# Performance work log

Hardware: AMD Instinct MI355X
Metric: run time of the kernel (lower is better)

The kernel has to match this reference:

```python
import jax, jax.numpy as jnp
import numpy as np

# ---- piecewise-linear surrogate tables (constants of the surrogate ops) ----
_N = 512
_GX = np.linspace(-10.0, 10.0, _N).astype(np.float32)
_GY = (0.5 * _GX * (1.0 + np.tanh(np.sqrt(2.0 / np.pi) * (_GX + 0.044715 * _GX ** 3)))).astype(np.float32)
_EX = np.linspace(-30.0, 0.0, _N).astype(np.float32)
_EY = np.exp(_EX).astype(np.float32)
_IX = np.geomspace(1e-3, 4096.0, _N).astype(np.float32)
_IY = (1.0 / _IX).astype(np.float32)
_RX = np.geomspace(1e-6, 100.0, _N).astype(np.float32)
_RY = (1.0 / np.sqrt(_RX)).astype(np.float32)

GX, GY = jnp.asarray(_GX), jnp.asarray(_GY)
EX, EY = jnp.asarray(_EX), jnp.asarray(_EY)
IX, IY = jnp.asarray(_IX), jnp.asarray(_IY)
RX, RY = jnp.asarray(_RX), jnp.asarray(_RY)

EXP_CLIP_MIN = -30.0
LN_EPS = 1e-5
N_HEAD = 16

pwl_gelu = lambda x: jnp.interp(x, GX, GY)
pwl_exp = lambda x: jnp.interp(x, EX, EY)
pwl_inv = lambda x: jnp.interp(x, IX, IY)
pwl_rsqrt = lambda x: jnp.interp(x, RX, RY)


def _layernorm_approx(x, w, b):
    mu = jnp.mean(x, axis=-1, keepdims=True)
    xc = x - mu
    var = jnp.mean(xc * xc, axis=-1, keepdims=True)
    inv_std = pwl_rsqrt(var + LN_EPS)
    return xc * inv_std * w + b


def _attn_approx(x, c_attn_w, c_attn_b, c_proj_w, c_proj_b):
    B, T, D = x.shape
    hd = D // N_HEAD
    scale = 1.0 / jnp.sqrt(jnp.float32(hd))
    qkv = x @ c_attn_w + c_attn_b                      # [B,T,3D]
    q, k, v = jnp.split(qkv, 3, axis=-1)
    q = q.reshape(B, T, N_HEAD, hd).transpose(0, 2, 1, 3)  # [B,H,T,hd]
    k = k.reshape(B, T, N_HEAD, hd).transpose(0, 2, 1, 3)
    v = v.reshape(B, T, N_HEAD, hd).transpose(0, 2, 1, 3)
    scores = jnp.einsum('bhqd,bhkd->bhqk', q, k) * scale    # [B,H,T,T]
    causal = jnp.tril(jnp.ones((T, T), dtype=bool))
    scores = jnp.where(causal, scores, -jnp.inf)
    m = jnp.max(scores, axis=-1, keepdims=True)
    s = jnp.clip(scores - m, EXP_CLIP_MIN, 0.0)             # masked -> -30
    e = pwl_exp(s)
    p = e * pwl_inv(jnp.sum(e, axis=-1, keepdims=True))
    out = jnp.einsum('bhqk,bhkd->bhqd', p, v)
    out = out.transpose(0, 2, 1, 3).reshape(B, T, D)
    return out @ c_proj_w + c_proj_b


def _mlp_approx(x, fc_w, fc_b, proj_w, proj_b):
    h = pwl_gelu(x @ fc_w + fc_b)
    return h @ proj_w + proj_b


def setup_inputs() -> dict:
    key = jax.random.key(0)
    ks = jax.random.split(key, 8)
    B, T, D = 2, 1024, 2048
    DF = 4 * D
    w = 0.02
    return {
        'x': jax.random.normal(ks[0], (B, T, D), jnp.float32),
        'ln_1_w': jnp.ones((D,), jnp.float32),
        'ln_1_b': jnp.zeros((D,), jnp.float32),
        'ln_2_w': jnp.ones((D,), jnp.float32),
        'ln_2_b': jnp.zeros((D,), jnp.float32),
        'c_attn_w': w * jax.random.normal(ks[1], (D, 3 * D), jnp.float32),
        'c_attn_b': jnp.zeros((3 * D,), jnp.float32),
        'c_proj_w': w * jax.random.normal(ks[2], (D, D), jnp.float32),
        'c_proj_b': jnp.zeros((D,), jnp.float32),
        'fc_w': w * jax.random.normal(ks[3], (D, DF), jnp.float32),
        'fc_b': jnp.zeros((DF,), jnp.float32),
        'proj_w': w * jax.random.normal(ks[4], (DF, D), jnp.float32),
        'proj_b': jnp.zeros((D,), jnp.float32),
    }


def reference(x, ln_1_w, ln_1_b, ln_2_w, ln_2_b, c_attn_w, c_attn_b,
              c_proj_w, c_proj_b, fc_w, fc_b, proj_w, proj_b):
    x = x + _attn_approx(_layernorm_approx(x, ln_1_w, ln_1_b),
                         c_attn_w, c_attn_b, c_proj_w, c_proj_b)
    x = x + _mlp_approx(_layernorm_approx(x, ln_2_w, ln_2_b),
                        fc_w, fc_b, proj_w, proj_b)
    return x
```

## Files before the change

### kernel.cpp

```cpp
#include <hip/hip_runtime.h>
#include <hip/hip_bf16.h>
#include <stdint.h>

typedef unsigned short u16;
typedef __bf16 bf16x8 __attribute__((ext_vector_type(8)));
typedef float f32x4 __attribute__((ext_vector_type(4)));
typedef u16 u16x8 __attribute__((ext_vector_type(8)));

#define MFMA16(a, b, c) __builtin_amdgcn_mfma_f32_16x16x32_bf16(a, b, c, 0, 0, 0)

typedef __attribute__((address_space(3))) unsigned as3_uint;
typedef __attribute__((address_space(1))) unsigned as1_uint;

__device__ __forceinline__ void gload_lds16(const void* g, void* l) {
  __builtin_amdgcn_global_load_lds((const as1_uint*)g, (as3_uint*)l, 16, 0, 0);
}

__device__ __forceinline__ u16 f2bf(float f) {
  unsigned u = __float_as_uint(f);
  u += 0x7FFF + ((u >> 16) & 1);
  return (u16)(u >> 16);
}

__device__ __forceinline__ float pwl_lin(float x, float x0, float x1, float invStep,
                                         const float* __restrict__ Bt,
                                         const float* __restrict__ Ct) {
  float xc = fminf(fmaxf(x, x0), x1);
  int i = (int)floorf((x - x0) * invStep);
  i = max(0, min(510, i));
  return fmaf(Bt[i], xc, Ct[i]);
}

__device__ __forceinline__ float pwl_log(float x, float x0, float x1, float lnx0, float invL,
                                         const float* __restrict__ Bt,
                                         const float* __restrict__ Ct) {
  float xc = fminf(fmaxf(x, x0), x1);
  int i = (int)floorf((logf(xc) - lnx0) * invL);
  i = max(0, min(510, i));
  return fmaf(Bt[i], xc, Ct[i]);
}

__global__ void init_tables(float* __restrict__ tb) {
  __shared__ float xs[4][512], ys[4][512];
  int i = threadIdx.x;
  if (i < 512) {
    double t = (double)i / 511.0;
    float xg = (float)(-10.0 + 20.0 * t);
    double xd = (double)xg;
    xs[0][i] = xg;
    ys[0][i] = (float)(0.5 * xd * (1.0 + tanh(0.7978845608028654 * (xd + 0.044715 * xd * xd * xd))));
    float xe = (float)(-30.0 + 30.0 * t);
    xs[1][i] = xe;
    ys[1][i] = (float)exp((double)xe);
    double li = -3.0 + t * (log10(4096.0) + 3.0);
    float xi = (float)pow(10.0, li);
    if (i == 0) xi = 1e-3f;
    if (i == 511) xi = 4096.0f;
    xs[2][i] = xi;
    ys[2][i] = 1.0f / xi;
    double lr = -6.0 + t * 8.0;
    float xr2 = (float)pow(10.0, lr);
    if (i == 0) xr2 = 1e-6f;
    if (i == 511) xr2 = 100.0f;
    xs[3][i] = xr2;
    ys[3][i] = 1.0f / sqrtf(xr2);
  }
  __syncthreads();
  if (i < 511) {
#pragma unroll
    for (int tc = 0; tc < 4; ++tc) {
      double bq = ((double)ys[tc][i + 1] - (double)ys[tc][i]) /
                  ((double)xs[tc][i + 1] - (double)xs[tc][i]);
      double cq = (double)ys[tc][i] - bq * (double)xs[tc][i];
      tb[tc * 1024 + i] = (float)bq;
      tb[tc * 1024 + 512 + i] = (float)cq;
    }
  }
}

__global__ __launch_bounds__(256) void ln_kernel(const float* __restrict__ x,
                                                 const float* __restrict__ w,
                                                 const float* __restrict__ b,
                                                 u16* __restrict__ out,
                                                 const float* __restrict__ tb) {
  int row = blockIdx.x, tid = threadIdx.x;
  const float4* xr = (const float4*)(x + (size_t)row * 2048);
  float4 v0 = xr[tid], v1 = xr[tid + 256];
  float s = ((v0.x + v0.y) + (v0.z + v0.w)) + ((v1.x + v1.y) + (v1.z + v1.w));
#pragma unroll
  for (int m = 32; m; m >>= 1) s += __shfl_xor(s, m, 64);
  __shared__ float red1[4], red2[4];
  int wv = tid >> 6;
  if ((tid & 63) == 0) red1[wv] = s;
  __syncthreads();
  float mu = (red1[0] + red1[1] + red1[2] + red1[3]) * (1.0f / 2048.0f);
  float a0 = v0.x - mu, a1 = v0.y - mu, a2 = v0.z - mu, a3 = v0.w - mu;
  float a4 = v1.x - mu, a5 = v1.y - mu, a6 = v1.z - mu, a7 = v1.w - mu;
  float q = ((a0 * a0 + a1 * a1) + (a2 * a2 + a3 * a3)) +
            ((a4 * a4 + a5 * a5) + (a6 * a6 + a7 * a7));
#pragma unroll
  for (int m = 32; m; m >>= 1) q += __shfl_xor(q, m, 64);
  if ((tid & 63) == 0) red2[wv] = q;
  __syncthreads();
  float var = (red2[0] + red2[1] + red2[2] + red2[3]) * (1.0f / 2048.0f);
  float istd = pwl_log(var + 1e-5f, 1e-6f, 100.0f, -13.8155106f, 27.7405655f, tb + 3072, tb + 3584);
  const float4* wr4 = (const float4*)w;
  const float4* br4 = (const float4*)b;
  float4 w0 = wr4[tid], w1 = wr4[tid + 256];
  float4 b0 = br4[tid], b1 = br4[tid + 256];
  u16 o0 = f2bf(fmaf(a0 * istd, w0.x, b0.x));
  u16 o1 = f2bf(fmaf(a1 * istd, w0.y, b0.y));
  u16 o2 = f2bf(fmaf(a2 * istd, w0.z, b0.z));
  u16 o3 = f2bf(fmaf(a3 * istd, w0.w, b0.w));
  u16 o4 = f2bf(fmaf(a4 * istd, w1.x, b1.x));
  u16 o5 = f2bf(fmaf(a5 * istd, w1.y, b1.y));
  u16 o6 = f2bf(fmaf(a6 * istd, w1.z, b1.z));
  u16 o7 = f2bf(fmaf(a7 * istd, w1.w, b1.w));
  uint2 p0, p1;
  p0.x = (unsigned)o0 | ((unsigned)o1 << 16);
  p0.y = (unsigned)o2 | ((unsigned)o3 << 16);
  p1.x = (unsigned)o4 | ((unsigned)o5 << 16);
  p1.y = (unsigned)o6 | ((unsigned)o7 << 16);
  uint2* orow = (uint2*)(out + (size_t)row * 2048);
  orow[tid] = p0;
  orow[tid + 256] = p1;
}

__global__ __launch_bounds__(256) void cast_transpose(const float* __restrict__ W,
                                                      u16* __restrict__ WT, int K, int N) {
  __shared__ u16 s[64][130];
  int j0 = blockIdx.x * 64, i0 = blockIdx.y * 128;
  int tid = threadIdx.x;
  int c = tid & 63, g = tid >> 6;
#pragma unroll
  for (int rr = g; rr < 128; rr += 4) {
    s[c][rr] = f2bf(W[(size_t)(i0 + rr) * N + j0 + c]);
  }
  __syncthreads();
  int r = tid >> 2;
  int cc0 = (tid & 3) * 32;
  unsigned* dst = (unsigned*)(WT + (size_t)(j0 + r) * K + i0 + cc0);
#pragma unroll
  for (int ii = 0; ii < 16; ++ii) {
    unsigned lo = s[r][cc0 + 2 * ii], hi = s[r][cc0 + 2 * ii + 1];
    dst[ii] = lo | (hi << 16);
  }
}

__global__ __launch_bounds__(256) void vtrans_kernel(const u16* __restrict__ qkv,
                                                     u16* __restrict__ vt) {
  int tt = blockIdx.x, dd = blockIdx.y, bh = blockIdx.z;
  int b = bh >> 4, h = bh & 15;
  __shared__ u16 s[64][72];
  int tid = threadIdx.x;
  const u16* src = qkv + ((size_t)b * 1024 + tt * 64) * 6144 + 4096 + h * 128 + dd * 64;
#pragma unroll
  for (int it = 0; it < 2; ++it) {
    int idx = it * 256 + tid;
    int r = idx >> 3, c = idx & 7;
    u16x8 v = *(const u16x8*)(src + (size_t)r * 6144 + c * 8);
#pragma unroll
    for (int j = 0; j < 8; ++j) s[r][c * 8 + j] = v[j];
  }
  __syncthreads();
  u16* dst = vt + ((size_t)bh * 128 + dd * 64) * 1024 + tt * 64;
#pragma unroll
  for (int it = 0; it < 2; ++it) {
    int idx = it * 256 + tid;
    int d = idx >> 3, c2 = idx & 7;
    u16x8 o;
#pragma unroll
    for (int j = 0; j < 8; ++j) o[j] = s[c2 * 8 + j][d];
    *(u16x8*)(dst + (size_t)d * 1024 + c2 * 8) = o;
  }
}

template <int EPI>
__global__ __launch_bounds__(256) void gemm_bt(const u16* __restrict__ A,
                                               const u16* __restrict__ BT,
                                               const float* __restrict__ bias,
                                               const float* __restrict__ add,
                                               float* __restrict__ outF,
                                               u16* __restrict__ outH, int M, int N, int K,
                                               const float* __restrict__ tb) {
  __shared__ u16 sA[128 * 32], sB[128 * 32];
  int tid = threadIdx.x, lane = tid & 63, w = tid >> 6;
  int l15 = lane & 15, lg = lane >> 4;
  int wr = w >> 1, wc = w & 1;
  int mBase = blockIdx.y * 128, nBase = blockIdx.x * 128;

  f32x4 acc[4][4] = {};

  int rowA = tid >> 2, chA = tid & 3;
  const u16* gA = A + (size_t)(mBase + rowA) * K + chA * 8;
  const u16* gB = BT + (size_t)(nBase + rowA) * K + chA * 8;
  u16* sAw = sA + w * 512;
  u16* sAw2 = sA + 2048 + w * 512;
  u16* sBw = sB + w * 512;
  u16* sBw2 = sB + 2048 + w * 512;
  size_t k64 = (size_t)64 * K;

  for (int k0 = 0; k0 < K; k0 += 32) {
    gload_lds16(gA + k0, sAw);
    gload_lds16(gA + k0 + k64, sAw2);
    gload_lds16(gB + k0, sBw);
    gload_lds16(gB + k0 + k64, sBw2);
    __syncthreads();
    bf16x8 aF[4], bF[4];
#pragma unroll
    for (int m = 0; m < 4; ++m)
      aF[m] = *(const bf16x8*)&sA[(wr * 64 + m * 16 + l15) * 32 + lg * 8];
#pragma unroll
    for (int n = 0; n < 4; ++n)
      bF[n] = *(const bf16x8*)&sB[(wc * 64 + n * 16 + l15) * 32 + lg * 8];
#pragma unroll
    for (int m = 0; m < 4; ++m)
#pragma unroll
      for (int n = 0; n < 4; ++n) acc[m][n] = MFMA16(aF[m], bF[n], acc[m][n]);
    __syncthreads();
  }

  float bv[4];
#pragma unroll
  for (int n = 0; n < 4; ++n) bv[n] = bias[nBase + wc * 64 + n * 16 + l15];
#pragma unroll
  for (int m = 0; m < 4; ++m) {
    int row0 = mBase + wr * 64 + m * 16 + lg * 4;
#pragma unroll
    for (int n = 0; n < 4; ++n) {
      int col = nBase + wc * 64 + n * 16 + l15;
#pragma unroll
      for (int r = 0; r < 4; ++r) {
        size_t oidx = (size_t)(row0 + r) * N + col;
        float v = acc[m][n][r] + bv[n];
        if (EPI == 1) {
          v += add[oidx];
          outF[oidx] = v;
        } else if (EPI == 2) {
          v = pwl_lin(v, -10.0f, 10.0f, 511.0f / 20.0f, tb, tb + 512);
          outH[oidx] = f2bf(v);
        } else {
          outH[oidx] = f2bf(v);
        }
      }
    }
  }
}

__global__ __launch_bounds__(256) void attn_kernel(const u16* __restrict__ qkv,
                                                   const u16* __restrict__ vt,
                                                   u16* __restrict__ outA,
                                                   const float* __restrict__ tb) {
  int bid = blockIdx.x;
  int qt = 15 - (bid >> 5);
  int bh = bid & 31;
  int b = bh >> 4, h = bh & 15;
  int tid = threadIdx.x, lane = tid & 63, w = tid >> 6;
  int l15 = lane & 15, lg = lane >> 4;

  __shared__ u16 sQ[64 * 128];
  __shared__ u16 sK[64 * 128];
  __shared__ u16 sVT[128 * 64];
  __shared__ __bf16 sP[4][16 * 72];

  const size_t RS = 6144;
  int q0 = qt * 64;
  const u16* qg = qkv + ((size_t)b * 1024 + q0) * RS + h * 128;
  const u16* kg = qkv + (size_t)b * 1024 * RS + 2048 + h * 128;
  const u16* vg = vt + (size_t)bh * 128 * 1024;
  int ntiles = qt + 1;
  const float scale = 0.08838834764831845f;
  const float* EB = tb + 1024;
  const float* EC = tb + 1536;

#pragma unroll
  for (int it = 0; it < 4; ++it) {
    int idx = it * 256 + tid;
    int r = idx >> 4, ch = idx & 15;
    gload_lds16(qg + (size_t)r * RS + (ch ^ (r & 7)) * 8, sQ + (size_t)(it * 256 + w * 64) * 8);
  }
  __syncthreads();

  bf16x8 aQ[4];
#pragma unroll
  for (int kk = 0; kk < 4; ++kk) {
    int row = w * 16 + l15;
    int off = (row * 256 + ((kk * 64 + lg * 16) ^ ((row & 7) << 4))) >> 1;
    aQ[kk] = *(const bf16x8*)&sQ[off];
  }

  float mrun[4], ssum[4];
#pragma unroll
  for (int r = 0; r < 4; ++r) {
    mrun[r] = -3.0e38f;
    ssum[r] = 0.f;
  }
  f32x4 oacc[8] = {};
  int qrow_w = q0 + w * 16;

  for (int t = 0; t < ntiles; ++t) {
    __syncthreads();
#pragma unroll
    for (int it = 0; it < 4; ++it) {
      int idx = it * 256 + tid;
      int r = idx >> 4, ch = idx & 15;
      gload_lds16(kg + (size_t)(t * 64 + r) * RS + (ch ^ (r & 7)) * 8,
                  sK + (size_t)(it * 256 + w * 64) * 8);
      int d = idx >> 3, c = idx & 7;
      gload_lds16(vg + (size_t)d * 1024 + t * 64 + (c ^ (d & 7)) * 8,
                  sVT + (size_t)(it * 256 + w * 64) * 8);
    }
    __syncthreads();

    f32x4 sc[4];
#pragma unroll
    for (int n = 0; n < 4; ++n) {
      sc[n] = (f32x4){0.f, 0.f, 0.f, 0.f};
#pragma unroll
      for (int kk = 0; kk < 4; ++kk) {
        int row = n * 16 + l15;
        int off = (row * 256 + ((kk * 64 + lg * 16) ^ ((row & 7) << 4))) >> 1;
        bf16x8 bK = *(const bf16x8*)&sK[off];
        sc[n] = MFMA16(aQ[kk], bK, sc[n]);
      }
    }

    float mt[4], sv[4][4];
#pragma unroll
    for (int r = 0; r < 4; ++r) mt[r] = -3.0e38f;
#pragma unroll
    for (int n = 0; n < 4; ++n)
#pragma unroll
      for (int r = 0; r < 4; ++r) {
        int key = t * 64 + n * 16 + l15;
        int qq = qrow_w + lg * 4 + r;
        float v = (key <= qq) ? sc[n][r] * scale : -3.0e38f;
        sv[n][r] = v;
        mt[r] = fmaxf(mt[r], v);
      }
#pragma unroll
    for (int m = 8; m; m >>= 1)
#pragma unroll
      for (int r = 0; r < 4; ++r) mt[r] = fmaxf(mt[r], __shfl_xor(mt[r], m, 64));

#pragma unroll
    for (int r = 0; r < 4; ++r) {
      float mn = fmaxf(mrun[r], mt[r]);
      float f = __expf(mrun[r] - mn);
      mrun[r] = mn;
      ssum[r] *= f;
#pragma unroll
      for (int fi = 0; fi < 8; ++fi) oacc[fi][r] *= f;
    }

#pragma unroll
    for (int n = 0; n < 4; ++n)
#pragma unroll
      for (int r = 0; r < 4; ++r) {
        float scv = fminf(fmaxf(sv[n][r] - mrun[r], -30.0f), 0.0f);
        float e = pwl_lin(scv, -30.0f, 0.0f, 511.0f / 30.0f, EB, EC);
        ssum[r] += e;
        sP[w][(lg * 4 + r) * 72 + n * 16 + l15] = (__bf16)e;
      }

#pragma unroll
    for (int kk = 0; kk < 2; ++kk) {
      bf16x8 aP = *(const bf16x8*)&sP[w][l15 * 72 + kk * 32 + lg * 8];
#pragma unroll
      for (int fi = 0; fi < 8; ++fi) {
        int d = fi * 16 + l15;
        int off = (d * 128 + ((kk * 64 + lg * 16) ^ ((d & 7) << 4))) >> 1;
        bf16x8 bV = *(const bf16x8*)&sVT[off];
        oacc[fi] = MFMA16(aP, bV, oacc[fi]);
      }
    }
  }

#pragma unroll
  for (int m = 8; m; m >>= 1)
#pragma unroll
    for (int r = 0; r < 4; ++r) ssum[r] += __shfl_xor(ssum[r], m, 64);

  int skipped = 1024 - ntiles * 64;
#pragma unroll
  for (int r = 0; r < 4; ++r) {
    float s = ssum[r] + (float)skipped * 9.357623e-14f;
    float inv = pwl_log(s, 1e-3f, 4096.0f, -6.9077553f, 33.5620689f, tb + 2048, tb + 2560);
    int qq = qrow_w + lg * 4 + r;
    size_t base = ((size_t)b * 1024 + qq) * 2048 + (size_t)h * 128;
#pragma unroll
    for (int fi = 0; fi < 8; ++fi) outA[base + fi * 16 + l15] = f2bf(oacc[fi][r] * inv);
  }
}

extern "C" void kernel_launch(void* const* d_in, const int* in_sizes, int n_in, void* d_out,
                              int out_size, void* d_ws, size_t ws_size, hipStream_t stream) {
  const float* x = (const float*)d_in[0];
  const float* ln1w = (const float*)d_in[1];
  const float* ln1b = (const float*)d_in[2];
  const float* ln2w = (const float*)d_in[3];
  const float* ln2b = (const float*)d_in[4];
  const float* attnW = (const float*)d_in[5];
  const float* attnB = (const float*)d_in[6];
  const float* projW = (const float*)d_in[7];
  const float* projB = (const float*)d_in[8];
  const float* fcW = (const float*)d_in[9];
  const float* fcB = (const float*)d_in[10];
  const float* proj2W = (const float*)d_in[11];
  const float* proj2B = (const float*)d_in[12];
  float* out = (float*)d_out;

  char* ws = (char*)d_ws;
  float* tb = (float*)ws;
  u16* WT = (u16*)(ws + 16384);
  u16* VT = WT;
  u16* ABUF = (u16*)(ws + 16384 + 33554432);
  u16* QBUF = (u16*)(ws + 16384 + 33554432 + 8388608);
  float* X1 = (float*)(ws + 16384 + 33554432 + 8388608 + 33554432);

  init_tables<<<1, 512, 0, stream>>>(tb);

  ln_kernel<<<2048, 256, 0, stream>>>(x, ln1w, ln1b, ABUF, tb);
  cast_transpose<<<dim3(6144 / 64, 2048 / 128), 256, 0, stream>>>(attnW, WT, 2048, 6144);
  gemm_bt<0><<<dim3(48, 16), 256, 0, stream>>>(ABUF, WT, attnB, nullptr, nullptr, QBUF, 2048,
                                               6144, 2048, tb);
  vtrans_kernel<<<dim3(16, 2, 32), 256, 0, stream>>>(QBUF, VT);
  attn_kernel<<<512, 256, 0, stream>>>(QBUF, VT, ABUF, tb);
  cast_transpose<<<dim3(2048 / 64, 2048 / 128), 256, 0, stream>>>(projW, WT, 2048, 2048);
  gemm_bt<1><<<dim3(16, 16), 256, 0, stream>>>(ABUF, WT, projB, x, X1, nullptr, 2048, 2048,
                                               2048, tb);
  ln_kernel<<<2048, 256, 0, stream>>>(X1, ln2w, ln2b, ABUF, tb);
  cast_transpose<<<dim3(8192 / 64, 2048 / 128), 256, 0, stream>>>(fcW, WT, 2048, 8192);
  gemm_bt<2><<<dim3(64, 16), 256, 0, stream>>>(ABUF, WT, fcB, nullptr, nullptr, QBUF, 2048,
                                               8192, 2048, tb);
  cast_transpose<<<dim3(2048 / 64, 8192 / 128), 256, 0, stream>>>(proj2W, WT, 8192, 2048);
  gemm_bt<1><<<dim3(16, 16), 256, 0, stream>>>(QBUF, WT, proj2B, X1, out, nullptr, 2048, 2048,
                                               8192, tb);
}
```

Baseline: 749.1 us.

## Split K across two wave groups in projection GEMMs with LDS reduction

```diff
diff --git a/kernel.cpp b/kernel.cpp
--- a/kernel.cpp
+++ b/kernel.cpp
@@ -247,6 +247,106 @@
   }
 }
 
+template <int EPI>
+__global__ __launch_bounds__(512) void gemm_bt_sk(const u16* __restrict__ A,
+                                                  const u16* __restrict__ BT,
+                                                  const float* __restrict__ bias,
+                                                  const float* __restrict__ add,
+                                                  float* __restrict__ outF,
+                                                  u16* __restrict__ outH, int M, int N, int K,
+                                                  const float* __restrict__ tb) {
+  __shared__ u16 smem[16384];
+  u16* sA = smem;
+  u16* sB = smem + 8192;
+  float* red = (float*)smem;
+
+  int tid = threadIdx.x, lane = tid & 63, w = tid >> 6;
+  int l15 = lane & 15, lg = lane >> 4;
+  int q = w & 3, grp = w >> 2;
+  int wr = q >> 1, wc = q & 1;
+  int mBase = blockIdx.y * 128, nBase = blockIdx.x * 128;
+  int Kh = K >> 1;
+
+  f32x4 acc[4][4] = {};
+
+  int ts = tid & 255;
+  int rowA = ts >> 2, chA = ts & 3;
+  const u16* gA = A + (size_t)(mBase + rowA) * K + (size_t)grp * Kh + chA * 8;
+  const u16* gB = BT + (size_t)(nBase + rowA) * K + (size_t)grp * Kh + chA * 8;
+  int w4 = w & 3;
+  u16* sAw = sA + grp * 4096 + w4 * 512;
+  u16* sAw2 = sA + grp * 4096 + 2048 + w4 * 512;
+  u16* sBw = sB + grp * 4096 + w4 * 512;
+  u16* sBw2 = sB + grp * 4096 + 2048 + w4 * 512;
+  size_t k64 = (size_t)64 * K;
+  const u16* sAr = sA + grp * 4096;
+  const u16* sBr = sB + grp * 4096;
+
+  for (int k0 = 0; k0 < Kh; k0 += 32) {
+    gload_lds16(gA + k0, sAw);
+    gload_lds16(gA + k0 + k64, sAw2);
+    gload_lds16(gB + k0, sBw);
+    gload_lds16(gB + k0 + k64, sBw2);
+    __syncthreads();
+    bf16x8 aF[4], bF[4];
+#pragma unroll
+    for (int m = 0; m < 4; ++m)
+      aF[m] = *(const bf16x8*)&sAr[(wr * 64 + m * 16 + l15) * 32 + lg * 8];
+#pragma unroll
+    for (int n = 0; n < 4; ++n)
+      bF[n] = *(const bf16x8*)&sBr[(wc * 64 + n * 16 + l15) * 32 + lg * 8];
+#pragma unroll
+    for (int m = 0; m < 4; ++m)
+#pragma unroll
+      for (int n = 0; n < 4; ++n) acc[m][n] = MFMA16(aF[m], bF[n], acc[m][n]);
+    __syncthreads();
+  }
+
+  float bv[4];
+#pragma unroll
+  for (int n = 0; n < 4; ++n) bv[n] = bias[nBase + wc * 64 + n * 16 + l15];
+
+#pragma unroll
+  for (int chunk = 0; chunk < 2; ++chunk) {
+    if (grp == 1) {
+#pragma unroll
+      for (int mm = 0; mm < 2; ++mm)
+#pragma unroll
+        for (int n = 0; n < 4; ++n)
+          *(f32x4*)(red + ((q * 8 + mm * 4 + n) << 8) + lane * 4) = acc[chunk * 2 + mm][n];
+    }
+    __syncthreads();
+    if (grp == 0) {
+#pragma unroll
+      for (int mm = 0; mm < 2; ++mm) {
+        int m = chunk * 2 + mm;
+        int row0 = mBase + wr * 64 + m * 16 + lg * 4;
+#pragma unroll
+        for (int n = 0; n < 4; ++n) {
+          f32x4 o = *(const f32x4*)(red + ((q * 8 + mm * 4 + n) << 8) + lane * 4);
+          f32x4 a = acc[m][n];
+          int col = nBase + wc * 64 + n * 16 + l15;
+#pragma unroll
+          for (int r = 0; r < 4; ++r) {
+            size_t oidx = (size_t)(row0 + r) * N + col;
+            float v = a[r] + o[r] + bv[n];
+            if (EPI == 1) {
+              v += add[oidx];
+              outF[oidx] = v;
+            } else if (EPI == 2) {
+              v = pwl_lin(v, -10.0f, 10.0f, 511.0f / 20.0f, tb, tb + 512);
+              outH[oidx] = f2bf(v);
+            } else {
+              outH[oidx] = f2bf(v);
+            }
+          }
+        }
+      }
+    }
+    __syncthreads();
+  }
+}
+
 __global__ __launch_bounds__(256) void attn_kernel(const u16* __restrict__ qkv,
                                                    const u16* __restrict__ vt,
                                                    u16* __restrict__ outA,
@@ -427,13 +527,13 @@
   vtrans_kernel<<<dim3(16, 2, 32), 256, 0, stream>>>(QBUF, VT);
   attn_kernel<<<512, 256, 0, stream>>>(QBUF, VT, ABUF, tb);
   cast_transpose<<<dim3(2048 / 64, 2048 / 128), 256, 0, stream>>>(projW, WT, 2048, 2048);
-  gemm_bt<1><<<dim3(16, 16), 256, 0, stream>>>(ABUF, WT, projB, x, X1, nullptr, 2048, 2048,
-                                               2048, tb);
+  gemm_bt_sk<1><<<dim3(16, 16), 512, 0, stream>>>(ABUF, WT, projB, x, X1, nullptr, 2048, 2048,
+                                                  2048, tb);
   ln_kernel<<<2048, 256, 0, stream>>>(X1, ln2w, ln2b, ABUF, tb);
   cast_transpose<<<dim3(8192 / 64, 2048 / 128), 256, 0, stream>>>(fcW, WT, 2048, 8192);
   gemm_bt<2><<<dim3(64, 16), 256, 0, stream>>>(ABUF, WT, fcB, nullptr, nullptr, QBUF, 2048,
                                                8192, 2048, tb);
   cast_transpose<<<dim3(2048 / 64, 8192 / 128), 256, 0, stream>>>(proj2W, WT, 8192, 2048);
-  gemm_bt<1><<<dim3(16, 16), 256, 0, stream>>>(QBUF, WT, proj2B, X1, out, nullptr, 2048, 2048,
-                                               8192, tb);
-}
+  gemm_bt_sk<1><<<dim3(16, 16), 512, 0, stream>>>(QBUF, WT, proj2B, X1, out, nullptr, 2048,
+                                                  2048, 8192, tb);
+}
```

After: 702.6 us. 1.07x faster.
